# Optimization experiments

Measured on AMD Instinct MI355X. Metric: run time of the kernel, lower is better.

Reference implementation:

```python
import jax, jax.numpy as jnp
import numpy as np

N_OBS = 8_000_000
N_CAM = 2_000
N_PTS = 1_000_000


def _rotate_quat(points, qt):
    """Rotate points by unit quaternion qt[...,:4]=(w,x,y,z), then translate by qt[...,4:7]."""
    q = qt[..., :4]
    q = q / jnp.linalg.norm(q, axis=-1, keepdims=True)
    w = q[..., :1]          # [N,1]
    v = q[..., 1:4]         # [N,3]
    # p' = p + 2*v x (v x p + w*p)
    t = jnp.cross(v, points) + w * points
    rotated = points + 2.0 * jnp.cross(v, t)
    return rotated + qt[..., 4:7]


def _project(points, camera_params):
    p = _rotate_quat(points, camera_params[..., :7])          # [N,3]
    proj = -p[..., :2] / p[..., 2:3]                          # perspective divide, [N,2]
    f = camera_params[..., 7:8]
    k1 = camera_params[..., 8:9]
    k2 = camera_params[..., 9:10]
    n = jnp.sum(proj * proj, axis=-1, keepdims=True)          # [N,1]
    r = 1.0 + k1 * n + k2 * n * n                             # radial distortion
    return proj * r * f


def setup_inputs() -> dict:
    key = jax.random.key(0)
    k1, k2, k3, k4, k5 = jax.random.split(key, 5)
    camera_params = jax.random.normal(k1, (N_CAM, 10), dtype=jnp.float32)
    # push translation z away from zero so the perspective divide is well-conditioned
    camera_params = camera_params.at[:, 6].add(5.0)
    points_3d = jax.random.normal(k2, (N_PTS, 3), dtype=jnp.float32)
    points_2d = jax.random.normal(k3, (N_OBS, 2), dtype=jnp.float32)
    camera_indices = jax.random.randint(k4, (N_OBS,), 0, N_CAM, dtype=jnp.int32)
    point_indices = jax.random.randint(k5, (N_OBS,), 0, N_PTS, dtype=jnp.int32)
    return {
        "points_2d": points_2d,
        "camera_indices": camera_indices,
        "point_indices": point_indices,
        "camera_params": camera_params,
        "points_3d": points_3d,
    }


def reference(points_2d, camera_indices, point_indices, camera_params, points_3d):
    pts = points_3d[point_indices]           # gather [N,3]
    cams = camera_params[camera_indices]     # gather [N,10]
    points_proj = _project(pts, cams)        # [N,2]
    return points_proj - points_2d
```

## Files before the change

kernel.cpp:

```cpp
#include <hip/hip_runtime.h>


typedef __attribute__((ext_vector_type(4))) float f32x4;
typedef __attribute__((ext_vector_type(2))) int   i32x2;

#define MAX_CAM_WORDS 20000

__device__ __forceinline__ float2 project_one(
    const float* lds_cams, int ci,
    float pxf, float pyf, float pzf,
    float obsx, float obsy)
{
    const float2* cl = reinterpret_cast<const float2*>(lds_cams + ci * 10);
    float2 c01 = cl[0];
    float2 c23 = cl[1];
    float2 c45 = cl[2];
    float2 c67 = cl[3];
    float2 c89 = cl[4];

    double px = (double)pxf, py = (double)pyf, pz = (double)pzf;
    double qw = (double)c01.x, qx = (double)c01.y;
    double qy = (double)c23.x, qz = (double)c23.y;

    double nrm2 = qw * qw + qx * qx + qy * qy + qz * qz;
    double s = 1.0 / sqrt(nrm2);
    double w  = qw * s;
    double vx = qx * s, vy = qy * s, vz = qz * s;

    double tx = (vy * pz - vz * py) + w * px;
    double ty = (vz * px - vx * pz) + w * py;
    double tz = (vx * py - vy * px) + w * pz;

    double X = (px + 2.0 * (vy * tz - vz * ty)) + (double)c45.x;
    double Y = (py + 2.0 * (vz * tx - vx * tz)) + (double)c45.y;
    double Z = (pz + 2.0 * (vx * ty - vy * tx)) + (double)c67.x;

    double rz  = 1.0 / Z;
    double prx = -X * rz;
    double pry = -Y * rz;

    double f  = (double)c67.y;
    double k1 = (double)c89.x, k2 = (double)c89.y;

    double nn = prx * prx + pry * pry;
    double r  = 1.0 + k1 * nn + k2 * nn * nn;
    double rf = r * f;

    float2 o;
    o.x = (float)(prx * rf - (double)obsx);
    o.y = (float)(pry * rf - (double)obsy);
    return o;
}

__global__ __launch_bounds__(1024, 8) void reproj_kernel(
    const f32x4*  __restrict__ p2d4,
    const int*    __restrict__ cam_idx,
    const int*    __restrict__ pt_idx,
    const float*  __restrict__ cams,
    const float*  __restrict__ pts,
    f32x4*        __restrict__ out4,
    int n, int ncam_words)
{
    __shared__ float lds_cams[MAX_CAM_WORDS];

    {
        int nv = ncam_words >> 2;
        if (nv > (MAX_CAM_WORDS >> 2)) nv = MAX_CAM_WORDS >> 2;
        const f32x4* src = reinterpret_cast<const f32x4*>(cams);
        f32x4* dst = reinterpret_cast<f32x4*>(lds_cams);
        for (int j = threadIdx.x; j < nv; j += blockDim.x)
            dst[j] = src[j];
        for (int j = (nv << 2) + threadIdx.x; j < ncam_words && j < MAX_CAM_WORDS;
             j += blockDim.x)
            lds_cams[j] = cams[j];
    }
    __syncthreads();

    int i = (blockIdx.x * blockDim.x + threadIdx.x) * 2;
    if (i + 1 < n) {
        i32x2 ci = __builtin_nontemporal_load(
            reinterpret_cast<const i32x2*>(cam_idx + i));
        i32x2 pi = __builtin_nontemporal_load(
            reinterpret_cast<const i32x2*>(pt_idx + i));
        f32x4 ob = __builtin_nontemporal_load(p2d4 + (i >> 1));

        const float* pA = pts + (size_t)pi.x * 3;
        const float* pB = pts + (size_t)pi.y * 3;
        float ax = pA[0], ay = pA[1], az = pA[2];
        float bx = pB[0], by = pB[1], bz = pB[2];

        float2 o0 = project_one(lds_cams, ci.x, ax, ay, az, ob.x, ob.y);
        float2 o1 = project_one(lds_cams, ci.y, bx, by, bz, ob.z, ob.w);
        f32x4 ov = {o0.x, o0.y, o1.x, o1.y};
        out4[i >> 1] = ov;
    } else if (i < n) {
        int ci = cam_idx[i];
        int pi = pt_idx[i];
        const float* pA = pts + (size_t)pi * 3;
        const float* p2 = reinterpret_cast<const float*>(p2d4);
        float2 o = project_one(lds_cams, ci, pA[0], pA[1], pA[2],
                               p2[2 * i], p2[2 * i + 1]);
        float* po = reinterpret_cast<float*>(out4);
        po[2 * i]     = o.x;
        po[2 * i + 1] = o.y;
    }
}

extern "C" void kernel_launch(void* const* d_in, const int* in_sizes, int n_in,
                              void* d_out, int out_size, void* d_ws, size_t ws_size,
                              hipStream_t stream) {
    const float* p2d     = (const float*)d_in[0];
    const int*   cam_idx = (const int*)d_in[1];
    const int*   pt_idx  = (const int*)d_in[2];
    const float* cams    = (const float*)d_in[3];
    const float* pts     = (const float*)d_in[4];

    int n   = in_sizes[1];
    int ncw = in_sizes[3];

    int threads = 1024;
    int per_block = threads * 2;
    int blocks = (n + per_block - 1) / per_block;

    reproj_kernel<<<blocks, threads, 0, stream>>>(
        (const f32x4*)p2d, cam_idx, pt_idx, cams, pts,
        (f32x4*)d_out, n, ncw);
}
```

Baseline: 140.1 us.

## Use persistent grid-stride loop with software-prefetched next iteration loads

Replaces the one-pair-per-thread launch with a fixed grid of at most 512 blocks that loop over the data with a grid stride. Each iteration issues the index, observation and point gather loads for the next pair before computing the current one, to overlap gather latency with the FP64 projection math. This also cuts the repeated per-block staging of the 80KB camera table into LDS, since far fewer blocks are launched. The cost is more live registers and possibly lower occupancy or latency hiding with only 512 blocks.

```diff
diff --git a/kernel.cpp b/kernel.cpp
--- a/kernel.cpp
+++ b/kernel.cpp
@@ -76,29 +76,62 @@
     }
     __syncthreads();
 
+    const int stride = gridDim.x * blockDim.x * 2;
     int i = (blockIdx.x * blockDim.x + threadIdx.x) * 2;
+
+    i32x2 ci, pi;
+    f32x4 ob;
+    float ax, ay, az, bx, by, bz;
     if (i + 1 < n) {
-        i32x2 ci = __builtin_nontemporal_load(
+        ci = __builtin_nontemporal_load(
             reinterpret_cast<const i32x2*>(cam_idx + i));
-        i32x2 pi = __builtin_nontemporal_load(
+        pi = __builtin_nontemporal_load(
             reinterpret_cast<const i32x2*>(pt_idx + i));
-        f32x4 ob = __builtin_nontemporal_load(p2d4 + (i >> 1));
-
+        ob = __builtin_nontemporal_load(p2d4 + (i >> 1));
         const float* pA = pts + (size_t)pi.x * 3;
         const float* pB = pts + (size_t)pi.y * 3;
-        float ax = pA[0], ay = pA[1], az = pA[2];
-        float bx = pB[0], by = pB[1], bz = pB[2];
+        ax = pA[0]; ay = pA[1]; az = pA[2];
+        bx = pB[0]; by = pB[1]; bz = pB[2];
+    }
+
+    while (i + 1 < n) {
+        int j = i + stride;
+
+        i32x2 cin, pin;
+        f32x4 obn;
+        float nax, nay, naz, nbx, nby, nbz;
+        bool nhave = (j + 1 < n);
+        if (nhave) {
+            cin = __builtin_nontemporal_load(
+                reinterpret_cast<const i32x2*>(cam_idx + j));
+            pin = __builtin_nontemporal_load(
+                reinterpret_cast<const i32x2*>(pt_idx + j));
+            obn = __builtin_nontemporal_load(p2d4 + (j >> 1));
+            const float* pA = pts + (size_t)pin.x * 3;
+            const float* pB = pts + (size_t)pin.y * 3;
+            nax = pA[0]; nay = pA[1]; naz = pA[2];
+            nbx = pB[0]; nby = pB[1]; nbz = pB[2];
+        }
 
         float2 o0 = project_one(lds_cams, ci.x, ax, ay, az, ob.x, ob.y);
         float2 o1 = project_one(lds_cams, ci.y, bx, by, bz, ob.z, ob.w);
         f32x4 ov = {o0.x, o0.y, o1.x, o1.y};
         out4[i >> 1] = ov;
-    } else if (i < n) {
-        int ci = cam_idx[i];
-        int pi = pt_idx[i];
-        const float* pA = pts + (size_t)pi * 3;
+
+        i = j;
+        if (nhave) {
+            ci = cin; pi = pin; ob = obn;
+            ax = nax; ay = nay; az = naz;
+            bx = nbx; by = nby; bz = nbz;
+        }
+    }
+
+    if (i < n) {
+        int cis = cam_idx[i];
+        int pis = pt_idx[i];
+        const float* pA = pts + (size_t)pis * 3;
         const float* p2 = reinterpret_cast<const float*>(p2d4);
-        float2 o = project_one(lds_cams, ci, pA[0], pA[1], pA[2],
+        float2 o = project_one(lds_cams, cis, pA[0], pA[1], pA[2],
                                p2[2 * i], p2[2 * i + 1]);
         float* po = reinterpret_cast<float*>(out4);
         po[2 * i]     = o.x;
@@ -119,8 +152,10 @@
     int ncw = in_sizes[3];
 
     int threads = 1024;
-    int per_block = threads * 2;
-    int blocks = (n + per_block - 1) / per_block;
+    int blocks = 512;
+    int need = (n + threads * 2 - 1) / (threads * 2);
+    if (need < blocks) blocks = need;
+    if (blocks < 1) blocks = 1;
 
     reproj_kernel<<<blocks, threads, 0, stream>>>(
         (const f32x4*)p2d, cam_idx, pt_idx, cams, pts,
```

Result: faster. 132.8 us (-5.2%).
